# Optimization experiments

Hardware: AMD Instinct MI355X
Metric: run time of the kernel (lower is better)

The kernel has to match this reference:

```python
import jax, jax.numpy as jnp
import numpy as np

B, T, I, H, C = 1024, 256, 14, 128, 1


def setup_inputs() -> dict:
    key = jax.random.key(0)
    ks = jax.random.split(key, 12)
    s = 1.0 / np.sqrt(H)  # torch nn.LSTM / nn.Linear uniform init bound
    u = lambda k, shp: jax.random.uniform(k, shp, jnp.float32, -s, s)
    return {
        "x": jax.random.normal(ks[0], (B, T, I), jnp.float32),
        # layer 0 (input_size -> hidden), gate order i,f,g,o stacked along first dim (4H)
        "w_ih0": u(ks[1], (4 * H, I)), "w_hh0": u(ks[2], (4 * H, H)),
        "b_ih0": u(ks[3], (4 * H,)), "b_hh0": u(ks[4], (4 * H,)),
        # layer 1 (hidden -> hidden)
        "w_ih1": u(ks[5], (4 * H, H)), "w_hh1": u(ks[6], (4 * H, H)),
        "b_ih1": u(ks[7], (4 * H,)), "b_hh1": u(ks[8], (4 * H,)),
        # final linear head
        "w_lin": u(ks[9], (C, H)), "b_lin": u(ks[10], (C,)),
    }


def _lstm_layer(x_seq, w_ih, w_hh, b_ih, b_hh):
    """Single LSTM layer, batch_first input [B,T,D] -> hidden sequence [B,T,H]."""
    Bb = x_seq.shape[0]
    Hh = w_hh.shape[1]
    # Hoist the input projection out of the recurrence: one big GEMM over all timesteps.
    x_proj = jnp.einsum('btd,gd->btg', x_seq, w_ih) + b_ih + b_hh  # [B,T,4H]
    x_proj = jnp.swapaxes(x_proj, 0, 1)  # [T,B,4H] for scan over time
    h0 = jnp.zeros((Bb, Hh), x_seq.dtype)
    c0 = jnp.zeros((Bb, Hh), x_seq.dtype)

    def step(carry, xp):
        h, c = carry
        gates = xp + h @ w_hh.T  # [B,4H]
        i, f, g, o = jnp.split(gates, 4, axis=-1)  # torch gate order: i,f,g,o
        i = jax.nn.sigmoid(i)
        f = jax.nn.sigmoid(f)
        g = jnp.tanh(g)
        o = jax.nn.sigmoid(o)
        c = f * c + i * g
        h = o * jnp.tanh(c)
        return (h, c), h

    _, hs = jax.lax.scan(step, (h0, c0), x_proj)  # hs: [T,B,H]
    return jnp.swapaxes(hs, 0, 1)  # [B,T,H]


def reference(x, w_ih0, w_hh0, b_ih0, b_hh0, w_ih1, w_hh1, b_ih1, b_hh1, w_lin, b_lin):
    h1 = _lstm_layer(x, w_ih0, w_hh0, b_ih0, b_hh0)
    # nn.LSTM dropout=0.1 applies between layers only in training mode; inference => identity
    h2 = _lstm_layer(h1, w_ih1, w_hh1, b_ih1, b_hh1)
    last = h2[:, -1, :]  # [B,H] final timestep
    return last @ w_lin.T + b_lin  # [B,1]
```

## Files before the change

### kernel.cpp

```cpp
#include <hip/hip_runtime.h>

typedef _Float16 half8 __attribute__((ext_vector_type(8)));
typedef float floatx4 __attribute__((ext_vector_type(4)));

#define T_STEPS 256
#define BB      16
#define NBLK    64
#define NTH     512

#define WHH0_H  0
#define WIH1_H  65536
#define WHH1_H  131072
#define WIH0_H  196608

__device__ __forceinline__ float sig_(float z)  { return __builtin_amdgcn_rcpf(1.f + __expf(-z)); }
__device__ __forceinline__ float tanh_(float z) { return 1.f - 2.f * __builtin_amdgcn_rcpf(1.f + __expf(2.f * z)); }

__global__ __launch_bounds__(256) void prep_weights(
    const float* __restrict__ w_ih0, const float* __restrict__ w_hh0,
    const float* __restrict__ w_ih1, const float* __restrict__ w_hh1,
    _Float16* __restrict__ wf)
{
    const int idx = blockIdx.x * 256 + threadIdx.x;
    const int l  = idx & 63;
    const int ks = (idx >> 6) & 3;
    const int gi = (idx >> 8) & 3;
    const int wv = (idx >> 10) & 7;
    const int row = gi * 128 + wv * 16 + (l & 15);
    const int kb  = ks * 32 + (l >> 4) * 8;
#pragma unroll
    for (int j = 0; j < 8; ++j) {
        wf[WHH0_H + idx * 8 + j] = (_Float16)w_hh0[row * 128 + kb + j];
        wf[WIH1_H + idx * 8 + j] = (_Float16)w_ih1[row * 128 + kb + j];
        wf[WHH1_H + idx * 8 + j] = (_Float16)w_hh1[row * 128 + kb + j];
    }
    if (ks == 0) {
        const int kb0 = (l >> 4) * 8;
        const int oi = ((wv * 4 + gi) * 64 + l) * 8;
#pragma unroll
        for (int j = 0; j < 8; ++j) {
            const int k = kb0 + j;
            wf[WIH0_H + oi + j] = (k < 14) ? (_Float16)w_ih0[row * 14 + k] : (_Float16)0.f;
        }
    }
}

__global__ __launch_bounds__(NTH) void lstm2_mfma(
    const float* __restrict__ x, const _Float16* __restrict__ wf,
    const float* __restrict__ b_ih0, const float* __restrict__ b_hh0,
    const float* __restrict__ b_ih1, const float* __restrict__ b_hh1,
    const float* __restrict__ w_lin, const float* __restrict__ b_lin,
    float* __restrict__ out)
{
    __shared__ __align__(16) _Float16 whh0_lds[65536];
    __shared__ __align__(16) _Float16 h1buf[2][BB][128];
    __shared__ __align__(16) _Float16 h2buf[2][BB][128];
    __shared__ __align__(16) _Float16 xlds[2][BB][32];

    const int tid  = threadIdx.x;
    const int l    = tid & 63;
    const int wv   = tid >> 6;
    const int lrow = l & 15;
    const int lk   = l >> 4;
    const int b0   = blockIdx.x * BB;

    {
        const floatx4* src = (const floatx4*)(wf + WHH0_H);
        floatx4* dst = (floatx4*)whh0_lds;
        for (int i = tid; i < 8192; i += NTH) dst[i] = src[i];
    }
    for (int i = tid; i < 1024; i += NTH) {
        ((unsigned*)h1buf[1])[i] = 0u;
        ((unsigned*)h2buf[1])[i] = 0u;
    }
    for (int i = tid; i < 512; i += NTH) ((unsigned*)xlds)[i] = 0u;

    const int xr = tid / 14, xc = tid - xr * 14;
    const bool xload = tid < 224;
    const float* xptr = xload ? (x + (size_t)(b0 + xr) * (T_STEPS * 14) + xc) : x;
    if (xload) xlds[0][xr][xc] = (_Float16)xptr[0];

    half8 wih1f[16], whh1f[16], wih0f[4];
    {
        const half8* wsf = (const half8*)wf;
#pragma unroll
        for (int gi = 0; gi < 4; ++gi) {
#pragma unroll
            for (int ks = 0; ks < 4; ++ks) {
                const int idx = ((wv * 4 + gi) * 4 + ks) * 64 + l;
                wih1f[gi * 4 + ks] = wsf[WIH1_H / 8 + idx];
                whh1f[gi * 4 + ks] = wsf[WHH1_H / 8 + idx];
            }
            wih0f[gi] = wsf[WIH0_H / 8 + (wv * 4 + gi) * 64 + l];
        }
    }

    float bias1[4], bias2[4];
#pragma unroll
    for (int gi = 0; gi < 4; ++gi) {
        const int col = gi * 128 + wv * 16 + lrow;
        bias1[gi] = b_ih0[col] + b_hh0[col];
        bias2[gi] = b_ih1[col] + b_hh1[col];
    }

    float c1[4] = {0.f, 0.f, 0.f, 0.f}, c2[4] = {0.f, 0.f, 0.f, 0.f};

    const int fragcol = lk * 16;
    const char* wbase = (const char*)whh0_lds + ((wv * 16) * 64 + l) * 16;

    __syncthreads();

#pragma unroll 2
    for (int t = 0; t < T_STEPS; ++t) {
        const int cur = t & 1, prv = cur ^ 1;

        float xnext = 0.f;
        if (xload && t < T_STEPS - 1) xnext = xptr[(t + 1) * 14];

        const char* h1rd = (const char*)h1buf[prv];
        const char* h2rd = (const char*)h2buf[prv];
        half8 h1p[4], h2p[4];
#pragma unroll
        for (int ks = 0; ks < 4; ++ks) {
            const int off = lrow * 256 + ((ks * 64 + fragcol) ^ ((lrow & 7) << 4));
            h1p[ks] = *(const half8*)(h1rd + off);
            h2p[ks] = *(const half8*)(h2rd + off);
        }
        half8 xa = *(const half8*)((const char*)xlds[cur] + lrow * 64 + fragcol);

        floatx4 acc1[4], acc2[4];
#pragma unroll
        for (int gi = 0; gi < 4; ++gi) {
            acc1[gi] = (floatx4){bias1[gi], bias1[gi], bias1[gi], bias1[gi]};
            acc1[gi] = __builtin_amdgcn_mfma_f32_16x16x32_f16(xa, wih0f[gi], acc1[gi], 0, 0, 0);
#pragma unroll
            for (int ks = 0; ks < 4; ++ks) {
                const half8 wb = *(const half8*)(wbase + (gi * 4 + ks) * 1024);
                acc1[gi] = __builtin_amdgcn_mfma_f32_16x16x32_f16(h1p[ks], wb, acc1[gi], 0, 0, 0);
            }
        }
#pragma unroll
        for (int gi = 0; gi < 4; ++gi) {
            acc2[gi] = (floatx4){bias2[gi], bias2[gi], bias2[gi], bias2[gi]};
#pragma unroll
            for (int ks = 0; ks < 4; ++ks)
                acc2[gi] = __builtin_amdgcn_mfma_f32_16x16x32_f16(h2p[ks], whh1f[gi * 4 + ks], acc2[gi], 0, 0, 0);
        }

        {
            char* h1wr = (char*)h1buf[cur];
#pragma unroll
            for (int r = 0; r < 4; ++r) {
                const float ig = sig_(acc1[0][r]);
                const float fg = sig_(acc1[1][r]);
                const float gg = tanh_(acc1[2][r]);
                const float og = sig_(acc1[3][r]);
                c1[r] = fg * c1[r] + ig * gg;
                const float hv = og * tanh_(c1[r]);
                const int b = lk * 4 + r;
                const int off = b * 256 + (((wv * 16 + lrow) * 2) ^ ((b & 7) << 4));
                *(_Float16*)(h1wr + off) = (_Float16)hv;
            }
        }

        __syncthreads();

        {
            const char* h1nrd = (const char*)h1buf[cur];
#pragma unroll
            for (int ks = 0; ks < 4; ++ks) {
                const int off = lrow * 256 + ((ks * 64 + fragcol) ^ ((lrow & 7) << 4));
                const half8 h1n = *(const half8*)(h1nrd + off);
#pragma unroll
                for (int gi = 0; gi < 4; ++gi)
                    acc2[gi] = __builtin_amdgcn_mfma_f32_16x16x32_f16(h1n, wih1f[gi * 4 + ks], acc2[gi], 0, 0, 0);
            }
        }

        {
            char* h2wr = (char*)h2buf[cur];
#pragma unroll
            for (int r = 0; r < 4; ++r) {
                const float ig = sig_(acc2[0][r]);
                const float fg = sig_(acc2[1][r]);
                const float gg = tanh_(acc2[2][r]);
                const float og = sig_(acc2[3][r]);
                c2[r] = fg * c2[r] + ig * gg;
                const float hv = og * tanh_(c2[r]);
                const int b = lk * 4 + r;
                const int off = b * 256 + (((wv * 16 + lrow) * 2) ^ ((b & 7) << 4));
                *(_Float16*)(h2wr + off) = (_Float16)hv;
            }
        }

        if (xload && t < T_STEPS - 1) xlds[prv][xr][xc] = (_Float16)xnext;

        __syncthreads();
    }

    if (tid < BB) {
        const char* hb = (const char*)h2buf[1];
        float acc = b_lin[0];
        for (int j = 0; j < 128; ++j) {
            const int off = tid * 256 + ((j * 2) ^ ((tid & 7) << 4));
            acc += w_lin[j] * (float)(*(const _Float16*)(hb + off));
        }
        out[b0 + tid] = acc;
    }
}

extern "C" void kernel_launch(void* const* d_in, const int* in_sizes, int n_in,
                              void* d_out, int out_size, void* d_ws, size_t ws_size,
                              hipStream_t stream) {
    (void)in_sizes; (void)n_in; (void)ws_size; (void)out_size;
    const float* x     = (const float*)d_in[0];
    const float* w_ih0 = (const float*)d_in[1];
    const float* w_hh0 = (const float*)d_in[2];
    const float* b_ih0 = (const float*)d_in[3];
    const float* b_hh0 = (const float*)d_in[4];
    const float* w_ih1 = (const float*)d_in[5];
    const float* w_hh1 = (const float*)d_in[6];
    const float* b_ih1 = (const float*)d_in[7];
    const float* b_hh1 = (const float*)d_in[8];
    const float* w_lin = (const float*)d_in[9];
    const float* b_lin = (const float*)d_in[10];
    float* out = (float*)d_out;
    _Float16* wf = (_Float16*)d_ws;

    hipLaunchKernelGGL(prep_weights, dim3(32), dim3(256), 0, stream,
                       w_ih0, w_hh0, w_ih1, w_hh1, wf);
    hipLaunchKernelGGL(lstm2_mfma, dim3(NBLK), dim3(NTH), 0, stream,
                       x, wf, b_ih0, b_hh0, b_ih1, b_hh1, w_lin, b_lin, out);
}
```

Baseline: 515.9 us.

## Split LSTM layers into producer/consumer blocks linked by a global ring buffer

Each batch group is now handled by two workgroups: one runs layer 0 and one runs layer 1. Layer-0 hidden states pass through a 16-slot ring buffer in global memory, with atomic flags providing backpressure and readiness signalling. All weights are held in registers, so the LDS copy of w_hh0 is dropped, and x is loaded directly into MFMA fragments with a repacked w_ih0 layout. This doubles the block count and overlaps the two layers in time, so each block's serial chain per step is shorter. The cost is cross-block spin-waiting through L2, and the scheme relies on all 128 blocks being co-resident.

```diff
diff --git a/kernel.cpp b/kernel.cpp
--- a/kernel.cpp
+++ b/kernel.cpp
@@ -5,13 +5,16 @@
 
 #define T_STEPS 256
 #define BB      16
-#define NBLK    64
 #define NTH     512
+#define RING_W  16
 
 #define WHH0_H  0
 #define WIH1_H  65536
 #define WHH1_H  131072
 #define WIH0_H  196608
+#define RING_H  229376
+#define FLAG_B  4653056
+#define FLAG_BYTES 16384
 
 __device__ __forceinline__ float sig_(float z)  { return __builtin_amdgcn_rcpf(1.f + __expf(-z)); }
 __device__ __forceinline__ float tanh_(float z) { return 1.f - 2.f * __builtin_amdgcn_rcpf(1.f + __expf(2.f * z)); }
@@ -35,177 +38,221 @@
         wf[WHH1_H + idx * 8 + j] = (_Float16)w_hh1[row * 128 + kb + j];
     }
     if (ks == 0) {
-        const int kb0 = (l >> 4) * 8;
+        const int lk = l >> 4;
         const int oi = ((wv * 4 + gi) * 64 + l) * 8;
 #pragma unroll
         for (int j = 0; j < 8; ++j) {
-            const int k = kb0 + j;
-            wf[WIH0_H + oi + j] = (k < 14) ? (_Float16)w_ih0[row * 14 + k] : (_Float16)0.f;
+            float v = 0.f;
+            if (lk == 0)                v = w_ih0[row * 14 + j];
+            else if (lk == 1 && j >= 2) v = w_ih0[row * 14 + 6 + j];
+            wf[WIH0_H + oi + j] = (_Float16)v;
         }
     }
 }
 
-__global__ __launch_bounds__(NTH) void lstm2_mfma(
+__global__ __launch_bounds__(NTH) void lstm2_pipe(
     const float* __restrict__ x, const _Float16* __restrict__ wf,
     const float* __restrict__ b_ih0, const float* __restrict__ b_hh0,
     const float* __restrict__ b_ih1, const float* __restrict__ b_hh1,
     const float* __restrict__ w_lin, const float* __restrict__ b_lin,
-    float* __restrict__ out)
+    float* __restrict__ out, char* __restrict__ wsb)
 {
-    __shared__ __align__(16) _Float16 whh0_lds[65536];
-    __shared__ __align__(16) _Float16 h1buf[2][BB][128];
-    __shared__ __align__(16) _Float16 h2buf[2][BB][128];
-    __shared__ __align__(16) _Float16 xlds[2][BB][32];
+    __shared__ __align__(16) _Float16 hbuf[2][BB * 128];
 
     const int tid  = threadIdx.x;
     const int l    = tid & 63;
     const int wv   = tid >> 6;
     const int lrow = l & 15;
     const int lk   = l >> 4;
-    const int b0   = blockIdx.x * BB;
-
-    {
-        const floatx4* src = (const floatx4*)(wf + WHH0_H);
-        floatx4* dst = (floatx4*)whh0_lds;
-        for (int i = tid; i < 8192; i += NTH) dst[i] = src[i];
-    }
-    for (int i = tid; i < 1024; i += NTH) {
-        ((unsigned*)h1buf[1])[i] = 0u;
-        ((unsigned*)h2buf[1])[i] = 0u;
-    }
-    for (int i = tid; i < 512; i += NTH) ((unsigned*)xlds)[i] = 0u;
-
-    const int xr = tid / 14, xc = tid - xr * 14;
-    const bool xload = tid < 224;
-    const float* xptr = xload ? (x + (size_t)(b0 + xr) * (T_STEPS * 14) + xc) : x;
-    if (xload) xlds[0][xr][xc] = (_Float16)xptr[0];
-
-    half8 wih1f[16], whh1f[16], wih0f[4];
-    {
-        const half8* wsf = (const half8*)wf;
+    const int bid  = blockIdx.x;
+    const int pos  = bid & 7;
+    const int role = (bid >> 3) & 1;
+    const int g    = (bid >> 4) * 8 + pos;
+    const int b0   = g * BB;
+
+    _Float16* ring = (_Float16*)wsb + RING_H + (size_t)g * RING_W * 2048;
+    int* flag_p = (int*)(wsb + FLAG_B) + g * 64;
+    int* flag_c = flag_p + 32;
+
+    for (int i = tid; i < 1024; i += NTH) ((unsigned*)hbuf[1])[i] = 0u;
+
+    const half8* wsf = (const half8*)wf;
+
+    if (role == 0) {
+        half8 whh0f[16], wih0f[4];
 #pragma unroll
         for (int gi = 0; gi < 4; ++gi) {
+#pragma unroll
+            for (int ks = 0; ks < 4; ++ks)
+                whh0f[gi * 4 + ks] = wsf[WHH0_H / 8 + ((wv * 4 + gi) * 4 + ks) * 64 + l];
+            wih0f[gi] = wsf[WIH0_H / 8 + (wv * 4 + gi) * 64 + l];
+        }
+        float bias1[4];
+#pragma unroll
+        for (int gi = 0; gi < 4; ++gi) {
+            const int col = gi * 128 + wv * 16 + lrow;
+            bias1[gi] = b_ih0[col] + b_hh0[col];
+        }
+        float c1[4] = {0.f, 0.f, 0.f, 0.f};
+
+        const int coff = (lk == 1) ? 6 : 0;
+        const float* xp = x + (size_t)(b0 + lrow) * (T_STEPS * 14) + coff;
+        float xr[8];
+#pragma unroll
+        for (int j = 0; j < 8; ++j) xr[j] = xp[j];
+        int seen_c = 0;
+        __syncthreads();
+
+        for (int t = 0; t < T_STEPS; ++t) {
+            const int cur = t & 1, prv = cur ^ 1;
+            half8 xh;
+#pragma unroll
+            for (int j = 0; j < 8; ++j) xh[j] = (_Float16)xr[j];
+            if (t + 1 < T_STEPS) {
+#pragma unroll
+                for (int j = 0; j < 8; ++j) xr[j] = xp[(t + 1) * 14 + j];
+            }
+            const char* hrd = (const char*)hbuf[prv];
+            half8 h1p[4];
+#pragma unroll
+            for (int ks = 0; ks < 4; ++ks) {
+                const int off = lrow * 256 + ((ks * 64 + lk * 16) ^ ((lrow & 7) << 4));
+                h1p[ks] = *(const half8*)(hrd + off);
+            }
+            floatx4 acc[4];
+#pragma unroll
+            for (int gi = 0; gi < 4; ++gi) {
+                acc[gi] = (floatx4){bias1[gi], bias1[gi], bias1[gi], bias1[gi]};
+                acc[gi] = __builtin_amdgcn_mfma_f32_16x16x32_f16(xh, wih0f[gi], acc[gi], 0, 0, 0);
+#pragma unroll
+                for (int ks = 0; ks < 4; ++ks)
+                    acc[gi] = __builtin_amdgcn_mfma_f32_16x16x32_f16(h1p[ks], whh0f[gi * 4 + ks], acc[gi], 0, 0, 0);
+            }
+            if (t >= RING_W && tid == 0) {
+                while (seen_c < t - (RING_W - 1)) {
+                    seen_c = __hip_atomic_load(flag_c, __ATOMIC_RELAXED, __HIP_MEMORY_SCOPE_AGENT);
+                    if (seen_c < t - (RING_W - 1)) __builtin_amdgcn_s_sleep(2);
+                }
+            }
+            __syncthreads();
+            char* hwr = (char*)hbuf[cur];
+            _Float16* rt = ring + (size_t)(t & (RING_W - 1)) * 2048;
+            const int u = wv * 16 + lrow;
+#pragma unroll
+            for (int r = 0; r < 4; ++r) {
+                const float ig = sig_(acc[0][r]);
+                const float fg = sig_(acc[1][r]);
+                const float gg = tanh_(acc[2][r]);
+                const float og = sig_(acc[3][r]);
+                c1[r] = fg * c1[r] + ig * gg;
+                const float hv = og * tanh_(c1[r]);
+                const int b = lk * 4 + r;
+                const _Float16 hh = (_Float16)hv;
+                *(_Float16*)(hwr + b * 256 + ((u * 2) ^ ((b & 7) << 4))) = hh;
+                rt[b * 128 + u] = hh;
+            }
+            __syncthreads();
+            if (tid == 0)
+                __hip_atomic_store(flag_p, t + 1, __ATOMIC_RELEASE, __HIP_MEMORY_SCOPE_AGENT);
+        }
+    } else {
+        half8 wih1f[16], whh1f[16];
+#pragma unroll
+        for (int gi = 0; gi < 4; ++gi)
 #pragma unroll
             for (int ks = 0; ks < 4; ++ks) {
                 const int idx = ((wv * 4 + gi) * 4 + ks) * 64 + l;
                 wih1f[gi * 4 + ks] = wsf[WIH1_H / 8 + idx];
                 whh1f[gi * 4 + ks] = wsf[WHH1_H / 8 + idx];
             }
-            wih0f[gi] = wsf[WIH0_H / 8 + (wv * 4 + gi) * 64 + l];
-        }
-    }
-
-    float bias1[4], bias2[4];
-#pragma unroll
-    for (int gi = 0; gi < 4; ++gi) {
-        const int col = gi * 128 + wv * 16 + lrow;
-        bias1[gi] = b_ih0[col] + b_hh0[col];
-        bias2[gi] = b_ih1[col] + b_hh1[col];
-    }
-
-    float c1[4] = {0.f, 0.f, 0.f, 0.f}, c2[4] = {0.f, 0.f, 0.f, 0.f};
-
-    const int fragcol = lk * 16;
-    const char* wbase = (const char*)whh0_lds + ((wv * 16) * 64 + l) * 16;
-
-    __syncthreads();
-
-#pragma unroll 2
-    for (int t = 0; t < T_STEPS; ++t) {
-        const int cur = t & 1, prv = cur ^ 1;
-
-        float xnext = 0.f;
-        if (xload && t < T_STEPS - 1) xnext = xptr[(t + 1) * 14];
-
-        const char* h1rd = (const char*)h1buf[prv];
-        const char* h2rd = (const char*)h2buf[prv];
-        half8 h1p[4], h2p[4];
-#pragma unroll
-        for (int ks = 0; ks < 4; ++ks) {
-            const int off = lrow * 256 + ((ks * 64 + fragcol) ^ ((lrow & 7) << 4));
-            h1p[ks] = *(const half8*)(h1rd + off);
-            h2p[ks] = *(const half8*)(h2rd + off);
-        }
-        half8 xa = *(const half8*)((const char*)xlds[cur] + lrow * 64 + fragcol);
-
-        floatx4 acc1[4], acc2[4];
+        float bias2[4];
 #pragma unroll
         for (int gi = 0; gi < 4; ++gi) {
-            acc1[gi] = (floatx4){bias1[gi], bias1[gi], bias1[gi], bias1[gi]};
-            acc1[gi] = __builtin_amdgcn_mfma_f32_16x16x32_f16(xa, wih0f[gi], acc1[gi], 0, 0, 0);
-#pragma unroll
-            for (int ks = 0; ks < 4; ++ks) {
-                const half8 wb = *(const half8*)(wbase + (gi * 4 + ks) * 1024);
-                acc1[gi] = __builtin_amdgcn_mfma_f32_16x16x32_f16(h1p[ks], wb, acc1[gi], 0, 0, 0);
-            }
-        }
-#pragma unroll
-        for (int gi = 0; gi < 4; ++gi) {
-            acc2[gi] = (floatx4){bias2[gi], bias2[gi], bias2[gi], bias2[gi]};
-#pragma unroll
-            for (int ks = 0; ks < 4; ++ks)
-                acc2[gi] = __builtin_amdgcn_mfma_f32_16x16x32_f16(h2p[ks], whh1f[gi * 4 + ks], acc2[gi], 0, 0, 0);
-        }
-
-        {
-            char* h1wr = (char*)h1buf[cur];
-#pragma unroll
-            for (int r = 0; r < 4; ++r) {
-                const float ig = sig_(acc1[0][r]);
-                const float fg = sig_(acc1[1][r]);
-                const float gg = tanh_(acc1[2][r]);
-                const float og = sig_(acc1[3][r]);
-                c1[r] = fg * c1[r] + ig * gg;
-                const float hv = og * tanh_(c1[r]);
-                const int b = lk * 4 + r;
-                const int off = b * 256 + (((wv * 16 + lrow) * 2) ^ ((b & 7) << 4));
-                *(_Float16*)(h1wr + off) = (_Float16)hv;
-            }
-        }
+            const int col = gi * 128 + wv * 16 + lrow;
+            bias2[gi] = b_ih1[col] + b_hh1[col];
+        }
+        float c2[4] = {0.f, 0.f, 0.f, 0.f};
+        int seen_p = 0;
+        const int toff = lrow * 128 + lk * 8;
 
         __syncthreads();
-
-        {
-            const char* h1nrd = (const char*)h1buf[cur];
-#pragma unroll
-            for (int ks = 0; ks < 4; ++ks) {
-                const int off = lrow * 256 + ((ks * 64 + fragcol) ^ ((lrow & 7) << 4));
-                const half8 h1n = *(const half8*)(h1nrd + off);
-#pragma unroll
-                for (int gi = 0; gi < 4; ++gi)
-                    acc2[gi] = __builtin_amdgcn_mfma_f32_16x16x32_f16(h1n, wih1f[gi * 4 + ks], acc2[gi], 0, 0, 0);
-            }
-        }
-
-        {
-            char* h2wr = (char*)h2buf[cur];
-#pragma unroll
-            for (int r = 0; r < 4; ++r) {
-                const float ig = sig_(acc2[0][r]);
-                const float fg = sig_(acc2[1][r]);
-                const float gg = tanh_(acc2[2][r]);
-                const float og = sig_(acc2[3][r]);
-                c2[r] = fg * c2[r] + ig * gg;
-                const float hv = og * tanh_(c2[r]);
-                const int b = lk * 4 + r;
-                const int off = b * 256 + (((wv * 16 + lrow) * 2) ^ ((b & 7) << 4));
-                *(_Float16*)(h2wr + off) = (_Float16)hv;
-            }
-        }
-
-        if (xload && t < T_STEPS - 1) xlds[prv][xr][xc] = (_Float16)xnext;
-
+        if (tid == 0) {
+            while (seen_p < 2) {
+                seen_p = __hip_atomic_load(flag_p, __ATOMIC_ACQUIRE, __HIP_MEMORY_SCOPE_AGENT);
+                if (seen_p < 2) __builtin_amdgcn_s_sleep(2);
+            }
+        }
         __syncthreads();
-    }
-
-    if (tid < BB) {
-        const char* hb = (const char*)h2buf[1];
-        float acc = b_lin[0];
-        for (int j = 0; j < 128; ++j) {
-            const int off = tid * 256 + ((j * 2) ^ ((tid & 7) << 4));
-            acc += w_lin[j] * (float)(*(const _Float16*)(hb + off));
-        }
-        out[b0 + tid] = acc;
+        half8 h1nA[4], h1nB[4];
+#pragma unroll
+        for (int ks = 0; ks < 4; ++ks) h1nA[ks] = *(const half8*)(ring + toff + ks * 32);
+#pragma unroll
+        for (int ks = 0; ks < 4; ++ks) h1nB[ks] = *(const half8*)(ring + 2048 + toff + ks * 32);
+
+#define CSTEP(T, H1N, CUR)                                                          \
+        {                                                                           \
+            const char* hrd = (const char*)hbuf[(CUR) ^ 1];                         \
+            half8 h2p[4];                                                           \
+            _Pragma("unroll")                                                       \
+            for (int ks = 0; ks < 4; ++ks) {                                        \
+                const int off = lrow * 256 + ((ks * 64 + lk * 16) ^ ((lrow & 7) << 4)); \
+                h2p[ks] = *(const half8*)(hrd + off);                               \
+            }                                                                       \
+            floatx4 acc[4];                                                         \
+            _Pragma("unroll")                                                       \
+            for (int gi = 0; gi < 4; ++gi) {                                        \
+                acc[gi] = (floatx4){bias2[gi], bias2[gi], bias2[gi], bias2[gi]};    \
+                _Pragma("unroll")                                                   \
+                for (int ks = 0; ks < 4; ++ks) {                                    \
+                    acc[gi] = __builtin_amdgcn_mfma_f32_16x16x32_f16(h2p[ks], whh1f[gi * 4 + ks], acc[gi], 0, 0, 0); \
+                    acc[gi] = __builtin_amdgcn_mfma_f32_16x16x32_f16(H1N[ks], wih1f[gi * 4 + ks], acc[gi], 0, 0, 0); \
+                }                                                                   \
+            }                                                                       \
+            char* hwr = (char*)hbuf[CUR];                                           \
+            const int u = wv * 16 + lrow;                                           \
+            _Pragma("unroll")                                                       \
+            for (int r = 0; r < 4; ++r) {                                           \
+                const float ig = sig_(acc[0][r]);                                   \
+                const float fg = sig_(acc[1][r]);                                   \
+                const float gg = tanh_(acc[2][r]);                                  \
+                const float og = sig_(acc[3][r]);                                   \
+                c2[r] = fg * c2[r] + ig * gg;                                       \
+                const float hv = og * tanh_(c2[r]);                                 \
+                const int b = lk * 4 + r;                                           \
+                *(_Float16*)(hwr + b * 256 + ((u * 2) ^ ((b & 7) << 4))) = (_Float16)hv; \
+            }                                                                       \
+            if ((T) < T_STEPS - 2 && tid == 0) {                                    \
+                while (seen_p < (T) + 3) {                                          \
+                    seen_p = __hip_atomic_load(flag_p, __ATOMIC_ACQUIRE, __HIP_MEMORY_SCOPE_AGENT); \
+                    if (seen_p < (T) + 3) __builtin_amdgcn_s_sleep(2);              \
+                }                                                                   \
+            }                                                                       \
+            __syncthreads();                                                        \
+            if ((T) < T_STEPS - 2) {                                                \
+                const _Float16* rt = ring + (size_t)((((T) + 2) & (RING_W - 1))) * 2048; \
+                _Pragma("unroll")                                                   \
+                for (int ks = 0; ks < 4; ++ks)                                      \
+                    H1N[ks] = *(const half8*)(rt + toff + ks * 32);                 \
+            }                                                                       \
+            if (tid == 0)                                                           \
+                __hip_atomic_store(flag_c, (T) + 2, __ATOMIC_RELAXED, __HIP_MEMORY_SCOPE_AGENT); \
+        }
+
+        for (int t = 0; t < T_STEPS; t += 2) {
+            CSTEP(t,     h1nA, 0);
+            CSTEP(t + 1, h1nB, 1);
+        }
+#undef CSTEP
+
+        if (tid < BB) {
+            const char* hb = (const char*)hbuf[1];
+            float acc = b_lin[0];
+            for (int j = 0; j < 128; ++j) {
+                const int off = tid * 256 + ((j * 2) ^ ((tid & 7) << 4));
+                acc += w_lin[j] * (float)(*(const _Float16*)(hb + off));
+            }
+            out[b0 + tid] = acc;
+        }
     }
 }
 
@@ -225,10 +272,12 @@
     const float* w_lin = (const float*)d_in[9];
     const float* b_lin = (const float*)d_in[10];
     float* out = (float*)d_out;
-    _Float16* wf = (_Float16*)d_ws;
-
+    char* wsb = (char*)d_ws;
+
+    hipMemsetAsync(wsb + FLAG_B, 0, FLAG_BYTES, stream);
     hipLaunchKernelGGL(prep_weights, dim3(32), dim3(256), 0, stream,
-                       w_ih0, w_hh0, w_ih1, w_hh1, wf);
-    hipLaunchKernelGGL(lstm2_mfma, dim3(NBLK), dim3(NTH), 0, stream,
-                       x, wf, b_ih0, b_hh0, b_ih1, b_hh1, w_lin, b_lin, out);
+                       w_ih0, w_hh0, w_ih1, w_hh1, (_Float16*)d_ws);
+    hipLaunchKernelGGL(lstm2_pipe, dim3(128), dim3(NTH), 0, stream,
+                       x, (_Float16*)d_ws, b_ih0, b_hh0, b_ih1, b_hh1,
+                       w_lin, b_lin, out, wsb);
 }
```

New measurement: 545.8 us. +5.8%, slower.

## Skew layer-2 one timestep behind layer-1 to use one barrier per step

Applied to the files above, without the earlier changes.

Layer 2 now runs one timestep behind layer 1, using triple-buffered hidden-state tiles. Both layers' work for a step then sits between a single barrier, replacing the two barriers per step that serialized layer 1 and layer 2. The x input is now read straight from global memory into registers, with lanes remapped to an overlapping column window, so the LDS staging of x goes away. The change also adds a launch-bounds occupancy hint, a waitcnt+barrier macro, and a parallel final linear reduction using lane shuffles. Costs are the extra LDS buffer, an epilogue step, and added register pressure from the prefetched x values.

```diff
diff --git a/kernel.cpp b/kernel.cpp
--- a/kernel.cpp
+++ b/kernel.cpp
@@ -5,8 +5,8 @@
 
 #define T_STEPS 256
 #define BB      16
+#define NTH     512
 #define NBLK    64
-#define NTH     512
 
 #define WHH0_H  0
 #define WIH1_H  65536
@@ -35,17 +35,47 @@
         wf[WHH1_H + idx * 8 + j] = (_Float16)w_hh1[row * 128 + kb + j];
     }
     if (ks == 0) {
-        const int kb0 = (l >> 4) * 8;
+        const int lk = l >> 4;
         const int oi = ((wv * 4 + gi) * 64 + l) * 8;
 #pragma unroll
         for (int j = 0; j < 8; ++j) {
-            const int k = kb0 + j;
-            wf[WIH0_H + oi + j] = (k < 14) ? (_Float16)w_ih0[row * 14 + k] : (_Float16)0.f;
+            float v = 0.f;
+            if (lk == 0)                v = w_ih0[row * 14 + j];
+            else if (lk == 1 && j >= 2) v = w_ih0[row * 14 + 6 + j];
+            wf[WIH0_H + oi + j] = (_Float16)v;
         }
     }
 }
 
-__global__ __launch_bounds__(NTH) void lstm2_mfma(
+#define BARRIER() do {                                          \
+    asm volatile("s_waitcnt lgkmcnt(0)" ::: "memory");          \
+    __builtin_amdgcn_s_barrier();                               \
+    __builtin_amdgcn_sched_barrier(0);                          \
+} while (0)
+
+#define READFRAG(DSTARR, SRC) do {                                              \
+    _Pragma("unroll")                                                           \
+    for (int ks = 0; ks < 4; ++ks) {                                            \
+        const int off = lrow * 256 + ((ks * 64 + lk * 16) ^ ((lrow & 7) << 4)); \
+        DSTARR[ks] = *(const half8*)((const char*)(SRC) + off);                 \
+    }                                                                           \
+} while (0)
+
+#define ACTWRITE(ACC, CST, DST) do {                                            \
+    _Pragma("unroll")                                                           \
+    for (int r = 0; r < 4; ++r) {                                               \
+        const float ig = sig_(ACC[0][r]);                                       \
+        const float fg = sig_(ACC[1][r]);                                       \
+        const float gg = tanh_(ACC[2][r]);                                      \
+        const float og = sig_(ACC[3][r]);                                       \
+        CST[r] = fg * CST[r] + ig * gg;                                         \
+        const float hv = og * tanh_(CST[r]);                                    \
+        const int b = lk * 4 + r;                                               \
+        *(_Float16*)((DST) + b * 256 + (((u * 2)) ^ ((b & 7) << 4))) = (_Float16)hv; \
+    }                                                                           \
+} while (0)
+
+__global__ __launch_bounds__(NTH, 2) void lstm2_fused3(
     const float* __restrict__ x, const _Float16* __restrict__ wf,
     const float* __restrict__ b_ih0, const float* __restrict__ b_hh0,
     const float* __restrict__ b_ih1, const float* __restrict__ b_hh1,
@@ -53,9 +83,8 @@
     float* __restrict__ out)
 {
     __shared__ __align__(16) _Float16 whh0_lds[65536];
-    __shared__ __align__(16) _Float16 h1buf[2][BB][128];
-    __shared__ __align__(16) _Float16 h2buf[2][BB][128];
-    __shared__ __align__(16) _Float16 xlds[2][BB][32];
+    __shared__ __align__(16) _Float16 h1s[3][BB * 128];
+    __shared__ __align__(16) _Float16 h2s[3][BB * 128];
 
     const int tid  = threadIdx.x;
     const int l    = tid & 63;
@@ -63,38 +92,30 @@
     const int lrow = l & 15;
     const int lk   = l >> 4;
     const int b0   = blockIdx.x * BB;
+    const int u    = wv * 16 + lrow;
 
     {
         const floatx4* src = (const floatx4*)(wf + WHH0_H);
         floatx4* dst = (floatx4*)whh0_lds;
         for (int i = tid; i < 8192; i += NTH) dst[i] = src[i];
     }
-    for (int i = tid; i < 1024; i += NTH) {
-        ((unsigned*)h1buf[1])[i] = 0u;
-        ((unsigned*)h2buf[1])[i] = 0u;
-    }
-    for (int i = tid; i < 512; i += NTH) ((unsigned*)xlds)[i] = 0u;
-
-    const int xr = tid / 14, xc = tid - xr * 14;
-    const bool xload = tid < 224;
-    const float* xptr = xload ? (x + (size_t)(b0 + xr) * (T_STEPS * 14) + xc) : x;
-    if (xload) xlds[0][xr][xc] = (_Float16)xptr[0];
-
+    for (int i = tid; i < 3072; i += NTH) {
+        ((unsigned*)h1s)[i] = 0u;
+        ((unsigned*)h2s)[i] = 0u;
+    }
+
+    const half8* wsf = (const half8*)wf;
     half8 wih1f[16], whh1f[16], wih0f[4];
-    {
-        const half8* wsf = (const half8*)wf;
-#pragma unroll
-        for (int gi = 0; gi < 4; ++gi) {
-#pragma unroll
-            for (int ks = 0; ks < 4; ++ks) {
-                const int idx = ((wv * 4 + gi) * 4 + ks) * 64 + l;
-                wih1f[gi * 4 + ks] = wsf[WIH1_H / 8 + idx];
-                whh1f[gi * 4 + ks] = wsf[WHH1_H / 8 + idx];
-            }
-            wih0f[gi] = wsf[WIH0_H / 8 + (wv * 4 + gi) * 64 + l];
-        }
-    }
-
+#pragma unroll
+    for (int gi = 0; gi < 4; ++gi) {
+#pragma unroll
+        for (int ks = 0; ks < 4; ++ks) {
+            const int idx = ((wv * 4 + gi) * 4 + ks) * 64 + l;
+            wih1f[gi * 4 + ks] = wsf[WIH1_H / 8 + idx];
+            whh1f[gi * 4 + ks] = wsf[WHH1_H / 8 + idx];
+        }
+        wih0f[gi] = wsf[WIH0_H / 8 + (wv * 4 + gi) * 64 + l];
+    }
     float bias1[4], bias2[4];
 #pragma unroll
     for (int gi = 0; gi < 4; ++gi) {
@@ -102,110 +123,95 @@
         bias1[gi] = b_ih0[col] + b_hh0[col];
         bias2[gi] = b_ih1[col] + b_hh1[col];
     }
-
     float c1[4] = {0.f, 0.f, 0.f, 0.f}, c2[4] = {0.f, 0.f, 0.f, 0.f};
 
-    const int fragcol = lk * 16;
-    const char* wbase = (const char*)whh0_lds + ((wv * 16) * 64 + l) * 16;
-
-    __syncthreads();
-
-#pragma unroll 2
+    const int coff = (lk == 1) ? 6 : 0;
+    const float* xp = x + (size_t)(b0 + lrow) * (T_STEPS * 14) + coff;
+    float xr[8];
+#pragma unroll
+    for (int j = 0; j < 8; ++j) xr[j] = xp[j];
+
+    const char* wbase = (const char*)whh0_lds + (wv * 1024 + l) * 16;
+
+    BARRIER();
+
+    int sa = 0, sb = 1, scc = 2;
     for (int t = 0; t < T_STEPS; ++t) {
-        const int cur = t & 1, prv = cur ^ 1;
-
-        float xnext = 0.f;
-        if (xload && t < T_STEPS - 1) xnext = xptr[(t + 1) * 14];
-
-        const char* h1rd = (const char*)h1buf[prv];
-        const char* h2rd = (const char*)h2buf[prv];
-        half8 h1p[4], h2p[4];
-#pragma unroll
-        for (int ks = 0; ks < 4; ++ks) {
-            const int off = lrow * 256 + ((ks * 64 + fragcol) ^ ((lrow & 7) << 4));
-            h1p[ks] = *(const half8*)(h1rd + off);
-            h2p[ks] = *(const half8*)(h2rd + off);
-        }
-        half8 xa = *(const half8*)((const char*)xlds[cur] + lrow * 64 + fragcol);
-
-        floatx4 acc1[4], acc2[4];
+        half8 xh;
+#pragma unroll
+        for (int j = 0; j < 8; ++j) xh[j] = (_Float16)xr[j];
+        if (t + 1 < T_STEPS) {
+#pragma unroll
+            for (int j = 0; j < 8; ++j) xr[j] = xp[(t + 1) * 14 + j];
+        }
+
+        half8 h1p[4];
+        READFRAG(h1p, h1s[scc]);
+
+        floatx4 acc1[4];
 #pragma unroll
         for (int gi = 0; gi < 4; ++gi) {
             acc1[gi] = (floatx4){bias1[gi], bias1[gi], bias1[gi], bias1[gi]};
-            acc1[gi] = __builtin_amdgcn_mfma_f32_16x16x32_f16(xa, wih0f[gi], acc1[gi], 0, 0, 0);
+            acc1[gi] = __builtin_amdgcn_mfma_f32_16x16x32_f16(xh, wih0f[gi], acc1[gi], 0, 0, 0);
 #pragma unroll
             for (int ks = 0; ks < 4; ++ks) {
                 const half8 wb = *(const half8*)(wbase + (gi * 4 + ks) * 1024);
                 acc1[gi] = __builtin_amdgcn_mfma_f32_16x16x32_f16(h1p[ks], wb, acc1[gi], 0, 0, 0);
             }
         }
+
+        if (t > 0) {
+            half8 h2p[4];
+            READFRAG(h2p, h2s[sb]);
+            floatx4 acc2[4];
+#pragma unroll
+            for (int gi = 0; gi < 4; ++gi) {
+                acc2[gi] = (floatx4){bias2[gi], bias2[gi], bias2[gi], bias2[gi]};
+#pragma unroll
+                for (int ks = 0; ks < 4; ++ks) {
+                    acc2[gi] = __builtin_amdgcn_mfma_f32_16x16x32_f16(h2p[ks], whh1f[gi * 4 + ks], acc2[gi], 0, 0, 0);
+                    acc2[gi] = __builtin_amdgcn_mfma_f32_16x16x32_f16(h1p[ks], wih1f[gi * 4 + ks], acc2[gi], 0, 0, 0);
+                }
+            }
+            ACTWRITE(acc2, c2, (char*)h2s[scc]);
+        }
+
+        ACTWRITE(acc1, c1, (char*)h1s[sa]);
+
+        BARRIER();
+        const int tmp = sa; sa = sb; sb = scc; scc = tmp;
+    }
+
+    {
+        half8 h1p[4], h2p[4];
+        READFRAG(h1p, h1s[scc]);
+        READFRAG(h2p, h2s[sb]);
+        floatx4 acc2[4];
 #pragma unroll
         for (int gi = 0; gi < 4; ++gi) {
             acc2[gi] = (floatx4){bias2[gi], bias2[gi], bias2[gi], bias2[gi]};
 #pragma unroll
-            for (int ks = 0; ks < 4; ++ks)
+            for (int ks = 0; ks < 4; ++ks) {
                 acc2[gi] = __builtin_amdgcn_mfma_f32_16x16x32_f16(h2p[ks], whh1f[gi * 4 + ks], acc2[gi], 0, 0, 0);
-        }
-
-        {
-            char* h1wr = (char*)h1buf[cur];
-#pragma unroll
-            for (int r = 0; r < 4; ++r) {
-                const float ig = sig_(acc1[0][r]);
-                const float fg = sig_(acc1[1][r]);
-                const float gg = tanh_(acc1[2][r]);
-                const float og = sig_(acc1[3][r]);
-                c1[r] = fg * c1[r] + ig * gg;
-                const float hv = og * tanh_(c1[r]);
-                const int b = lk * 4 + r;
-                const int off = b * 256 + (((wv * 16 + lrow) * 2) ^ ((b & 7) << 4));
-                *(_Float16*)(h1wr + off) = (_Float16)hv;
+                acc2[gi] = __builtin_amdgcn_mfma_f32_16x16x32_f16(h1p[ks], wih1f[gi * 4 + ks], acc2[gi], 0, 0, 0);
             }
         }
-
-        __syncthreads();
-
-        {
-            const char* h1nrd = (const char*)h1buf[cur];
-#pragma unroll
-            for (int ks = 0; ks < 4; ++ks) {
-                const int off = lrow * 256 + ((ks * 64 + fragcol) ^ ((lrow & 7) << 4));
-                const half8 h1n = *(const half8*)(h1nrd + off);
-#pragma unroll
-                for (int gi = 0; gi < 4; ++gi)
-                    acc2[gi] = __builtin_amdgcn_mfma_f32_16x16x32_f16(h1n, wih1f[gi * 4 + ks], acc2[gi], 0, 0, 0);
-            }
-        }
-
-        {
-            char* h2wr = (char*)h2buf[cur];
-#pragma unroll
-            for (int r = 0; r < 4; ++r) {
-                const float ig = sig_(acc2[0][r]);
-                const float fg = sig_(acc2[1][r]);
-                const float gg = tanh_(acc2[2][r]);
-                const float og = sig_(acc2[3][r]);
-                c2[r] = fg * c2[r] + ig * gg;
-                const float hv = og * tanh_(c2[r]);
-                const int b = lk * 4 + r;
-                const int off = b * 256 + (((wv * 16 + lrow) * 2) ^ ((b & 7) << 4));
-                *(_Float16*)(h2wr + off) = (_Float16)hv;
-            }
-        }
-
-        if (xload && t < T_STEPS - 1) xlds[prv][xr][xc] = (_Float16)xnext;
-
-        __syncthreads();
-    }
-
-    if (tid < BB) {
-        const char* hb = (const char*)h2buf[1];
-        float acc = b_lin[0];
-        for (int j = 0; j < 128; ++j) {
-            const int off = tid * 256 + ((j * 2) ^ ((tid & 7) << 4));
-            acc += w_lin[j] * (float)(*(const _Float16*)(hb + off));
-        }
-        out[b0 + tid] = acc;
+        ACTWRITE(acc2, c2, (char*)h2s[scc]);
+        BARRIER();
+    }
+
+    if (tid < 64) {
+        const char* hb = (const char*)h2s[0];
+        const int bb = tid & 15, q = tid >> 4;
+        float acc = 0.f;
+#pragma unroll
+        for (int j5 = 0; j5 < 32; ++j5) {
+            const int j = q * 32 + j5;
+            acc += w_lin[j] * (float)(*(const _Float16*)(hb + bb * 256 + ((j * 2) ^ ((bb & 7) << 4))));
+        }
+        acc += __shfl_xor(acc, 16, 64);
+        acc += __shfl_xor(acc, 32, 64);
+        if (q == 0) out[b0 + bb] = acc + b_lin[0];
     }
 }
 
@@ -225,10 +231,10 @@
     const float* w_lin = (const float*)d_in[9];
     const float* b_lin = (const float*)d_in[10];
     float* out = (float*)d_out;
-    _Float16* wf = (_Float16*)d_ws;
 
     hipLaunchKernelGGL(prep_weights, dim3(32), dim3(256), 0, stream,
-                       w_ih0, w_hh0, w_ih1, w_hh1, wf);
-    hipLaunchKernelGGL(lstm2_mfma, dim3(NBLK), dim3(NTH), 0, stream,
-                       x, wf, b_ih0, b_hh0, b_ih1, b_hh1, w_lin, b_lin, out);
+                       w_ih0, w_hh0, w_ih1, w_hh1, (_Float16*)d_ws);
+    hipLaunchKernelGGL(lstm2_fused3, dim3(NBLK), dim3(NTH), 0, stream,
+                       x, (const _Float16*)d_ws, b_ih0, b_hh0, b_ih1, b_hh1,
+                       w_lin, b_lin, out);
 }
```

New measurement: 621.9 us. +20.6%, slower.
